# Kernel optimization log

Measured on AMD Instinct MI355X. Metric: run time of the kernel, lower is better.

## Reference

```python
import jax, jax.numpy as jnp
import numpy as np
import math

B, T, D, N = 4, 1024, 768, 7  # batch, seq, d_model, n_chambers
STEP, WARMUP = 4000, 2000      # curriculum: step past warmup -> all masks ~1
INIT_SCALE = 0.01


def _curriculum_masks():
    # NautilusScheduler.get_masks: smooth sigmoid activation per chamber (static floats)
    slope = 8.0 * N / WARMUP
    return [1.0 / (1.0 + math.exp(-slope * (STEP - WARMUP * (i + 0.5) / N))) for i in range(N)]


def _layernorm(x, g, b, eps=1e-5):
    m = jnp.mean(x, axis=-1, keepdims=True)
    v = jnp.mean((x - m) ** 2, axis=-1, keepdims=True)
    return (x - m) * jax.lax.rsqrt(v + eps) * g + b


def _chamber(h, Wq, Wk, gw, gb, sp, mask_val, causal):
    # get_bias stand-in: bilinear content bias (B,T,T)
    q = h @ Wq                                   # (B,T,D)
    k = h @ Wk                                   # (B,T,D)
    bias = jnp.einsum('btd,bsd->bts', q, k) / jnp.sqrt(jnp.asarray(D, h.dtype))
    bias = jnp.where(causal[None], bias, -jnp.inf)   # causal masked_fill
    w = jnp.nan_to_num(jax.nn.softmax(bias, axis=-1))
    enrichment = jnp.einsum('bts,bsd->btd', w, h) - h
    gate = jax.nn.sigmoid(h @ gw[:, None] + gb)      # (B,T,1)
    scale = jax.nn.softplus(sp)                      # learnable positive scale
    return scale * gate * mask_val * enrichment


def setup_inputs() -> dict:
    key = jax.random.key(0)
    ks = jax.random.split(key, 8)
    x = jax.random.normal(ks[0], (B, T, D), jnp.float32)
    s = 1.0 / np.sqrt(D)
    Wq = jax.random.normal(ks[1], (N, D, D), jnp.float32) * s
    Wk = jax.random.normal(ks[2], (N, D, D), jnp.float32) * s
    gate_w = jax.random.normal(ks[3], (N, D), jnp.float32) * 0.02
    gate_b = jnp.zeros((N,), jnp.float32)
    # per-chamber softplus-inverse init: log(exp(init*(1+3*prog))-1+1e-6)
    sp = np.array([math.log(math.exp(INIT_SCALE * (1.0 + 3.0 * i / (N - 1))) - 1.0 + 1e-6)
                   for i in range(N)], dtype=np.float32)
    scale_p = jnp.asarray(sp)
    merge_W = jax.random.normal(ks[4], (D, N * D), jnp.float32) * (1.0 / np.sqrt(N * D))
    return {
        'x': x, 'Wq': Wq, 'Wk': Wk, 'gate_w': gate_w, 'gate_b': gate_b,
        'scale_p': scale_p, 'merge_W': merge_W,
        'mode_logit': jnp.float32(0.0), 'residual_gate': jnp.float32(0.1),
        'ln_pre_g': jnp.ones((D,), jnp.float32), 'ln_pre_b': jnp.zeros((D,), jnp.float32),
        'ln_post_g': jnp.ones((D,), jnp.float32), 'ln_post_b': jnp.zeros((D,), jnp.float32),
    }


def reference(x, Wq, Wk, gate_w, gate_b, scale_p, merge_W, mode_logit,
              residual_gate, ln_pre_g, ln_pre_b, ln_post_g, ln_post_b):
    masks = _curriculum_masks()
    causal = jnp.tril(jnp.ones((T, T), bool))
    h = _layernorm(x, ln_pre_g, ln_pre_b)
    mode_gate = jax.nn.sigmoid(mode_logit)
    seq = jnp.zeros_like(h)
    deltas = []
    for i in range(N):  # fixed small structural loop over chambers
        seq = seq + _chamber(h + seq, Wq[i], Wk[i], gate_w[i], gate_b[i],
                             scale_p[i], masks[i], causal)
        deltas.append(_chamber(h, Wq[i], Wk[i], gate_w[i], gate_b[i],
                               scale_p[i], masks[i], causal))
    par = jnp.concatenate(deltas, axis=-1) @ merge_W.T  # (B,T,D)
    enrichment = (1.0 - mode_gate) * seq + mode_gate * par
    enrichment = _layernorm(enrichment, ln_post_g, ln_post_b)
    return x + residual_gate * enrichment
```

## Files before the change

### kernel.cpp

```cpp
#include <hip/hip_runtime.h>
#include <hip/hip_bf16.h>
#include <math.h>

#define D_MODEL 768
#define T_SEQ   1024
#define BATCH   4
#define NCH     7
#define ROWS    4096
#define KM      (NCH * D_MODEL)

typedef unsigned short u16;
typedef __attribute__((ext_vector_type(8))) short bh8;
typedef __attribute__((ext_vector_type(4))) float f32x4;

__device__ __forceinline__ u16 f2bf(float f) {
    union { float f; unsigned u; } v; v.f = f;
    return (u16)((v.u + 0x7fffu + ((v.u >> 16) & 1u)) >> 16);
}
__device__ __forceinline__ float bf2f(u16 b) {
    union { unsigned u; float f; } v; v.u = ((unsigned)b) << 16;
    return v.f;
}
__device__ __forceinline__ float wred_sum(float v) {
    #pragma unroll
    for (int o = 32; o; o >>= 1) v += __shfl_down(v, o, 64);
    return v;
}
__device__ __forceinline__ float wred_max(float v) {
    #pragma unroll
    for (int o = 32; o; o >>= 1) v = fmaxf(v, __shfl_down(v, o, 64));
    return v;
}
__device__ __forceinline__ float chamber_mask(int i) {
    float slope = 8.0f * 7.0f / 2000.0f;
    return 1.0f / (1.0f + __expf(-slope * (4000.0f - 2000.0f * (i + 0.5f) / 7.0f)));
}

#define GLD16(g, l) __builtin_amdgcn_global_load_lds( \
    (const __attribute__((address_space(1))) void*)(g), \
    (__attribute__((address_space(3))) void*)(l), 16, 0, 0)

__global__ __launch_bounds__(256)
void gemm_nt_kernel(const u16* __restrict__ A, const u16* __restrict__ B,
                    void* __restrict__ Cv,
                    int K, int lda, int ldb, int ldc,
                    long long sA1, long long sA2, long long sB1, long long sB2,
                    long long sC1, long long sC2, int zm,
                    float alpha, int mode, int causal_skip, int causal_k,
                    int kss, int klen)
{
    int bn = blockIdx.x, bm = blockIdx.y, bz = blockIdx.z;
    if (causal_skip && bn > bm) return;
    int bz1 = bz % zm, bz2 = bz / zm;

    const u16* Ab = A + bz1 * sA1 + bz2 * sA2 + (long long)(bm * 128) * lda;
    const u16* Bb = B + bz1 * sB1 + bz2 * sB2 + (long long)(bn * 128) * ldb;

    __shared__ u16 sm[4 * 128 * 32];
    u16* Al0 = sm;
    u16* Bl0 = sm + 128 * 32;
    u16* Al1 = sm + 2 * 128 * 32;
    u16* Bl1 = sm + 3 * 128 * 32;

    int tid  = threadIdx.x;
    int lane = tid & 63;
    int wave = tid >> 6;
    int wm = wave >> 1, wn = wave & 1;

    int k_begin = kss ? bz1 * kss : 0;
    int k_end   = klen ? (k_begin + klen) : K;
    if (causal_k) k_end = min(k_end, (bm + 1) * 128);

    f32x4 acc[4][4];
    #pragma unroll
    for (int i = 0; i < 4; i++)
        #pragma unroll
        for (int j = 0; j < 4; j++)
            acc[i][j] = (f32x4){0.f, 0.f, 0.f, 0.f};

    int srow = lane >> 2;
    int skq  = (lane & 3) * 8;
    int fm   = lane & 15;
    int fk   = (lane >> 4) * 8;

    for (int k0 = k_begin; k0 < k_end; k0 += 64) {
        __syncthreads();
        #pragma unroll
        for (int r = 0; r < 2; r++) {
            int row = r * 64 + wave * 16 + srow;
            long long ra = (long long)row * lda + k0 + skq;
            long long rb2 = (long long)row * ldb + k0 + skq;
            GLD16(Ab + ra,      Al0 + row * 32 + skq);
            GLD16(Bb + rb2,     Bl0 + row * 32 + skq);
            GLD16(Ab + ra + 32, Al1 + row * 32 + skq);
            GLD16(Bb + rb2 + 32, Bl1 + row * 32 + skq);
        }
        __syncthreads();

        #pragma unroll
        for (int p = 0; p < 2; p++) {
            const u16* Al = p ? Al1 : Al0;
            const u16* Bl = p ? Bl1 : Bl0;
            bh8 af[4], bf[4];
            #pragma unroll
            for (int i = 0; i < 4; i++)
                af[i] = *(const bh8*)(Al + (wm * 64 + i * 16 + fm) * 32 + fk);
            #pragma unroll
            for (int j = 0; j < 4; j++)
                bf[j] = *(const bh8*)(Bl + (wn * 64 + j * 16 + fm) * 32 + fk);
            #pragma unroll
            for (int i = 0; i < 4; i++)
                #pragma unroll
                for (int j = 0; j < 4; j++)
                    acc[i][j] = __builtin_amdgcn_mfma_f32_16x16x32_bf16(af[i], bf[j], acc[i][j], 0, 0, 0);
        }
    }

    int rbase = bm * 128 + wm * 64 + (lane >> 4) * 4;
    int cbase = bn * 128 + wn * 64 + (lane & 15);
    long long zoff = bz1 * sC1 + bz2 * sC2;
    if (mode == 1) {
        u16* C = (u16*)Cv + zoff;
        #pragma unroll
        for (int i = 0; i < 4; i++)
            #pragma unroll
            for (int j = 0; j < 4; j++)
                #pragma unroll
                for (int r = 0; r < 4; r++)
                    C[(long long)(rbase + i * 16 + r) * ldc + cbase + j * 16] = f2bf(acc[i][j][r] * alpha);
    } else if (mode == 3) {
        u16* C = (u16*)Cv + zoff;
        #pragma unroll
        for (int i = 0; i < 4; i++)
            #pragma unroll
            for (int j = 0; j < 4; j++)
                #pragma unroll
                for (int r = 0; r < 4; r++) {
                    union { _Float16 h; u16 u; } cv;
                    cv.h = (_Float16)(acc[i][j][r] * alpha);
                    C[(long long)(rbase + i * 16 + r) * ldc + cbase + j * 16] = cv.u;
                }
    } else {
        float* C = (float*)Cv + zoff;
        #pragma unroll
        for (int i = 0; i < 4; i++)
            #pragma unroll
            for (int j = 0; j < 4; j++)
                #pragma unroll
                for (int r = 0; r < 4; r++)
                    C[(long long)(rbase + i * 16 + r) * ldc + cbase + j * 16] = acc[i][j][r] * alpha;
    }
}

__global__ __launch_bounds__(256)
void gemm64_nt_kernel(const u16* __restrict__ A, const u16* __restrict__ B,
                      void* __restrict__ Cv,
                      int K, int lda, int ldb, int ldc,
                      long long sA1, long long sA2, long long sB1, long long sB2,
                      long long sC1, long long sC2, int zm,
                      float alpha, int mode, int causal_skip, int causal_k,
                      float* __restrict__ hhfp, const float* __restrict__ coefp,
                      u16* __restrict__ hbsp, u16* __restrict__ htsp,
                      const float* __restrict__ hp, u16* __restrict__ dbp)
{
    int bn = blockIdx.x, bm = blockIdx.y, bz = blockIdx.z;
    if (causal_skip && bn > bm) return;
    int bz1 = bz % zm, bz2 = bz / zm;

    const u16* Ab = A + bz1 * sA1 + bz2 * sA2 + (long long)(bm * 64) * lda;
    const u16* Bb = B + bz1 * sB1 + bz2 * sB2 + (long long)(bn * 64) * ldb;

    __shared__ u16 sm[4 * 64 * 32];
    u16* Al0 = sm;
    u16* Bl0 = sm + 64 * 32;
    u16* Al1 = sm + 2 * 64 * 32;
    u16* Bl1 = sm + 3 * 64 * 32;

    int tid  = threadIdx.x;
    int lane = tid & 63;
    int wave = tid >> 6;

    int k_end = causal_k ? min(K, (bm + 1) * 64) : K;

    f32x4 acc[4];
    #pragma unroll
    for (int j = 0; j < 4; j++) acc[j] = (f32x4){0.f, 0.f, 0.f, 0.f};

    int srow   = tid >> 2;
    int schunk = (tid & 3) * 8;
    int fm     = lane & 15;
    int fk     = (lane >> 4) * 8;

    for (int k0 = 0; k0 < k_end; k0 += 64) {
        __syncthreads();
        {
            long long ra  = (long long)srow * lda + k0 + schunk;
            long long rb2 = (long long)srow * ldb + k0 + schunk;
            GLD16(Ab + ra,       Al0 + srow * 32 + schunk);
            GLD16(Bb + rb2,      Bl0 + srow * 32 + schunk);
            GLD16(Ab + ra + 32,  Al1 + srow * 32 + schunk);
            GLD16(Bb + rb2 + 32, Bl1 + srow * 32 + schunk);
        }
        __syncthreads();

        #pragma unroll
        for (int p = 0; p < 2; p++) {
            const u16* Al = p ? Al1 : Al0;
            const u16* Bl = p ? Bl1 : Bl0;
            bh8 af = *(const bh8*)(Al + (wave * 16 + fm) * 32 + fk);
            bh8 bf[4];
            #pragma unroll
            for (int j = 0; j < 4; j++)
                bf[j] = *(const bh8*)(Bl + (j * 16 + fm) * 32 + fk);
            #pragma unroll
            for (int j = 0; j < 4; j++)
                acc[j] = __builtin_amdgcn_mfma_f32_16x16x32_bf16(af, bf[j], acc[j], 0, 0, 0);
        }
    }

    int rbase = bm * 64 + wave * 16 + (lane >> 4) * 4;
    int cbase = bn * 64 + (lane & 15);
    long long zoff = bz1 * sC1 + bz2 * sC2;
    if (mode == 1) {
        u16* C = (u16*)Cv + zoff;
        #pragma unroll
        for (int j = 0; j < 4; j++)
            #pragma unroll
            for (int r = 0; r < 4; r++)
                C[(long long)(rbase + r) * ldc + cbase + j * 16] = f2bf(acc[j][r] * alpha);
    } else if (mode == 3) {
        u16* C = (u16*)Cv + zoff;
        #pragma unroll
        for (int j = 0; j < 4; j++)
            #pragma unroll
            for (int r = 0; r < 4; r++) {
                union { _Float16 h; u16 u; } cv;
                cv.h = (_Float16)(acc[j][r] * alpha);
                C[(long long)(rbase + r) * ldc + cbase + j * 16] = cv.u;
            }
    } else if (mode == 5) {
        int b = bz1, ch = bz2;
        #pragma unroll
        for (int r = 0; r < 4; r++) {
            int t = rbase + r;
            long long rowg = (long long)b * T_SEQ + t;
            float cf = coefp[(long long)ch * ROWS + rowg];
            #pragma unroll
            for (int j = 0; j < 4; j++) {
                int d = cbase + j * 16;
                float hv = hp[rowg * D_MODEL + d];
                dbp[rowg * KM + ch * D_MODEL + d] = f2bf(cf * (acc[j][r] - hv));
            }
        }
    } else if (mode == 6) {
        __syncthreads();
        u16* tile = sm;
        #pragma unroll
        for (int r = 0; r < 4; r++) {
            int t = rbase + r;
            long long rowg = (long long)bz1 * T_SEQ + t;
            float cf = coefp[rowg];
            int tl = t - bm * 64;
            #pragma unroll
            for (int j = 0; j < 4; j++) {
                int d = cbase + j * 16;
                long long idx = rowg * D_MODEL + d;
                float v = hhfp[idx];
                float nh = v + cf * (acc[j][r] - v);
                hhfp[idx] = nh;
                u16 w = f2bf(nh);
                hbsp[idx] = w;
                tile[((lane & 15) + j * 16) * 66 + tl] = w;
            }
        }
        __syncthreads();
        int dl = tid >> 2, tch = (tid & 3) * 16;
        long long ob = (long long)bz1 * T_SEQ * D_MODEL +
                       (long long)(bn * 64 + dl) * T_SEQ + bm * 64 + tch;
        #pragma unroll
        for (int kk = 0; kk < 16; kk++)
            htsp[ob + kk] = tile[dl * 66 + tch + kk];
    } else {
        float* C = (float*)Cv + zoff;
        #pragma unroll
        for (int j = 0; j < 4; j++)
            #pragma unroll
            for (int r = 0; r < 4; r++)
                C[(long long)(rbase + r) * ldc + cbase + j * 16] = acc[j][r] * alpha;
    }
}

__global__ __launch_bounds__(256)
void ln_pre_kernel(const float* __restrict__ x, const float* __restrict__ g,
                   const float* __restrict__ b, float* __restrict__ h,
                   float* __restrict__ hhf, u16* __restrict__ hbp,
                   u16* __restrict__ hbs)
{
    int row = blockIdx.x;
    long long base = (long long)row * D_MODEL;
    int tid = threadIdx.x, lane = tid & 63, wave = tid >> 6;
    __shared__ float red[4];
    float v[3]; float s = 0.f;
    #pragma unroll
    for (int k = 0; k < 3; k++) { v[k] = x[base + tid + k * 256]; s += v[k]; }
    s = wred_sum(s);
    if (lane == 0) red[wave] = s;
    __syncthreads();
    float mean = (red[0] + red[1] + red[2] + red[3]) * (1.f / D_MODEL);
    __syncthreads();
    float sq = 0.f;
    #pragma unroll
    for (int k = 0; k < 3; k++) { float dd = v[k] - mean; sq += dd * dd; }
    sq = wred_sum(sq);
    if (lane == 0) red[wave] = sq;
    __syncthreads();
    float var = (red[0] + red[1] + red[2] + red[3]) * (1.f / D_MODEL);
    float rstd = rsqrtf(var + 1e-5f);
    #pragma unroll
    for (int k = 0; k < 3; k++) {
        int c = tid + k * 256;
        float o = (v[k] - mean) * rstd * g[c] + b[c];
        h[base + c] = o; hhf[base + c] = o;
        u16 w = f2bf(o);
        hbp[base + c] = w; hbs[base + c] = w;
    }
}

__global__ __launch_bounds__(256)
void transpose2_kernel(const u16* __restrict__ hb, u16* __restrict__ htp,
                       u16* __restrict__ hts)
{
    __shared__ u16 tile[32][33];
    int b = blockIdx.z;
    int d0 = blockIdx.x * 32, t0 = blockIdx.y * 32;
    int tx = threadIdx.x & 31, ty = threadIdx.x >> 5;
    long long bb = (long long)b * T_SEQ * D_MODEL;
    #pragma unroll
    for (int i = 0; i < 32; i += 8)
        tile[ty + i][tx] = hb[bb + (long long)(t0 + ty + i) * D_MODEL + d0 + tx];
    __syncthreads();
    #pragma unroll
    for (int i = 0; i < 32; i += 8) {
        long long o = bb + (long long)(d0 + ty + i) * T_SEQ + t0 + tx;
        u16 w = tile[tx][ty + i];
        htp[o] = w; hts[o] = w;
    }
}

__device__ __forceinline__ void softmax_row(u16* row, int len, int tid, int lane, int wave,
                                            float* red)
{
    float ev[4];
    float m = -3.0e38f;
    #pragma unroll
    for (int k = 0; k < 4; k++) {
        int s = tid + k * 256;
        if (s < len) {
            union { u16 u; _Float16 h; } cv; cv.u = row[s];
            ev[k] = (float)cv.h;
        } else ev[k] = -3.0e38f;
        m = fmaxf(m, ev[k]);
    }
    m = wred_max(m);
    if (lane == 0) red[wave] = m;
    __syncthreads();
    m = fmaxf(fmaxf(red[0], red[1]), fmaxf(red[2], red[3]));
    __syncthreads();
    float sum = 0.f;
    #pragma unroll
    for (int k = 0; k < 4; k++) {
        int s = tid + k * 256;
        float e = (s < len) ? __expf(ev[k] - m) : 0.f;
        ev[k] = e; sum += e;
    }
    sum = wred_sum(sum);
    if (lane == 0) red[wave] = sum;
    __syncthreads();
    sum = red[0] + red[1] + red[2] + red[3];
    float inv = 1.f / sum;
    #pragma unroll
    for (int k = 0; k < 4; k++)
        row[tid + k * 256] = f2bf(ev[k] * inv);
}

__global__ __launch_bounds__(256)
void softmax_kernel(u16* __restrict__ SP)
{
    int t = blockIdx.x, z = blockIdx.y;
    __shared__ float red[4];
    int tid = threadIdx.x, lane = tid & 63, wave = tid >> 6;
    softmax_row(SP + (long long)z * T_SEQ * T_SEQ + (long long)t * T_SEQ,
                t + 1, tid, lane, wave, red);
}

__global__ __launch_bounds__(256)
void softmax_coef_kernel(u16* __restrict__ SP, const float* __restrict__ hhf,
                         const float* __restrict__ gw, const float* __restrict__ gb,
                         const float* __restrict__ sp, int ci,
                         float* __restrict__ coefS)
{
    int t = blockIdx.x, z = blockIdx.y;
    int tid = threadIdx.x, lane = tid & 63, wave = tid >> 6;
    if (z == BATCH) {
        int row = t * 4 + wave;
        long long base = (long long)row * D_MODEL;
        const float* g = gw + ci * D_MODEL;
        float dot = 0.f;
        #pragma unroll
        for (int k = 0; k < 12; k++) dot += hhf[base + lane + 64 * k] * g[lane + 64 * k];
        dot = wred_sum(dot);
        if (lane == 0) {
            float gate = 1.f / (1.f + __expf(-(dot + gb[ci])));
            coefS[row] = log1pf(expf(sp[ci])) * chamber_mask(ci) * gate;
        }
        return;
    }
    __shared__ float red[4];
    softmax_row(SP + (long long)z * T_SEQ * T_SEQ + (long long)t * T_SEQ,
                t + 1, tid, lane, wave, red);
}

__global__ __launch_bounds__(256)
void coef_par_kernel(const float* __restrict__ h, const float* __restrict__ gw,
                     const float* __restrict__ gb, const float* __restrict__ sp,
                     float* __restrict__ coefP)
{
    int row = blockIdx.x * 4 + (threadIdx.x >> 6);
    int lane = threadIdx.x & 63;
    long long base = (long long)row * D_MODEL;
    float hv[12];
    #pragma unroll
    for (int k = 0; k < 12; k++) hv[k] = h[base + lane + 64 * k];
    for (int ci = 0; ci < NCH; ci++) {
        const float* g = gw + ci * D_MODEL;
        float dot = 0.f;
        #pragma unroll
        for (int k = 0; k < 12; k++) dot += hv[k] * g[lane + 64 * k];
        dot = wred_sum(dot);
        if (lane == 0) {
            float gate = 1.f / (1.f + __expf(-(dot + gb[ci])));
            coefP[ci * ROWS + row] = log1pf(expf(sp[ci])) * chamber_mask(ci) * gate;
        }
    }
}

__global__ __launch_bounds__(256)
void cast4_kernel(const float4* __restrict__ in, ushort4* __restrict__ outp, int n4)
{
    int i = blockIdx.x * 256 + threadIdx.x;
    if (i < n4) {
        float4 v = in[i];
        ushort4 o;
        o.x = f2bf(v.x); o.y = f2bf(v.y); o.z = f2bf(v.z); o.w = f2bf(v.w);
        outp[i] = o;
    }
}

__global__ __launch_bounds__(256)
void final_kernel(const float* __restrict__ x, const float* __restrict__ h,
                  const float* __restrict__ hhf, const u16* __restrict__ Pp,
                  const float* __restrict__ mode_logit, const float* __restrict__ residual_gate,
                  const float* __restrict__ g, const float* __restrict__ b,
                  float* __restrict__ out)
{
    const long long RDe = (long long)ROWS * D_MODEL;
    int row = blockIdx.x;
    long long base = (long long)row * D_MODEL;
    int tid = threadIdx.x, lane = tid & 63, wave = tid >> 6;
    __shared__ float red[4];
    float mg = 1.f / (1.f + __expf(-mode_logit[0]));
    float rg = residual_gate[0];
    float e[3]; float s = 0.f;
    #pragma unroll
    for (int k = 0; k < 3; k++) {
        int c = tid + k * 256;
        float p = 0.f;
        #pragma unroll
        for (int z = 0; z < NCH; z++) p += bf2f(Pp[z * RDe + base + c]);
        float v = (1.f - mg) * (hhf[base + c] - h[base + c]) + mg * p;
        e[k] = v; s += v;
    }
    s = wred_sum(s);
    if (lane == 0) red[wave] = s;
    __syncthreads();
    float mean = (red[0] + red[1] + red[2] + red[3]) * (1.f / D_MODEL);
    __syncthreads();
    float sq = 0.f;
    #pragma unroll
    for (int k = 0; k < 3; k++) { float dd = e[k] - mean; sq += dd * dd; }
    sq = wred_sum(sq);
    if (lane == 0) red[wave] = sq;
    __syncthreads();
    float var = (red[0] + red[1] + red[2] + red[3]) * (1.f / D_MODEL);
    float rstd = rsqrtf(var + 1e-5f);
    #pragma unroll
    for (int k = 0; k < 3; k++) {
        int c = tid + k * 256;
        out[base + c] = x[base + c] + rg * ((e[k] - mean) * rstd * g[c] + b[c]);
    }
}

extern "C" void kernel_launch(void* const* d_in, const int* in_sizes, int n_in,
                              void* d_out, int out_size, void* d_ws, size_t ws_size,
                              hipStream_t stream)
{
    (void)in_sizes; (void)n_in; (void)out_size; (void)ws_size;
    const float* x             = (const float*)d_in[0];
    const float* Wq            = (const float*)d_in[1];
    const float* Wk            = (const float*)d_in[2];
    const float* gate_w        = (const float*)d_in[3];
    const float* gate_b        = (const float*)d_in[4];
    const float* scale_p       = (const float*)d_in[5];
    const float* merge_W       = (const float*)d_in[6];
    const float* mode_logit    = (const float*)d_in[7];
    const float* residual_gate = (const float*)d_in[8];
    const float* ln_pre_g      = (const float*)d_in[9];
    const float* ln_pre_b      = (const float*)d_in[10];
    const float* ln_post_g     = (const float*)d_in[11];
    const float* ln_post_b     = (const float*)d_in[12];
    float* out = (float*)d_out;

    const long long DD  = (long long)D_MODEL * D_MODEL;
    const long long TD  = (long long)T_SEQ * D_MODEL;
    const long long TTs = (long long)T_SEQ * T_SEQ;
    const long long RDe = (long long)ROWS * D_MODEL;

    size_t off = 0;
    char* wsb = (char*)d_ws;
    auto alloc = [&](size_t bytes) -> void* {
        void* p = wsb + off; off += (bytes + 255) & ~(size_t)255; return p;
    };
    u16*   Mtb  = (u16*)alloc((size_t)NCH * DD * 2);
    u16*   mgb  = (u16*)alloc((size_t)D_MODEL * KM * 2);
    float* h    = (float*)alloc(RDe * 4);
    float* hhf  = (float*)alloc(RDe * 4);
    u16*   hbp  = (u16*)alloc(RDe * 2);
    u16*   htp  = (u16*)alloc(RDe * 2);
    u16*   hbs  = (u16*)alloc(RDe * 2);
    u16*   hts0 = (u16*)alloc(RDe * 2);
    u16*   hts1 = (u16*)alloc(RDe * 2);
    u16*   Spar = (u16*)alloc((size_t)(NCH * BATCH) * TTs * 2);
    u16*   Sseq = (u16*)alloc((size_t)BATCH * TTs * 2);
    u16*   Upar = (u16*)alloc((size_t)NCH * RDe * 2);
    u16*   Useq = (u16*)alloc(RDe * 2);
    u16*   db   = (u16*)alloc((size_t)ROWS * KM * 2);
    float* coefP= (float*)alloc((size_t)NCH * ROWS * 4);
    float* coefS= (float*)alloc((size_t)ROWS * 4);
    u16*   Wqb  = Spar;
    u16*   Wkb  = Spar + (size_t)NCH * DD;
    u16*   Pp   = Upar;

    const float sc = 1.0f / sqrtf((float)D_MODEL);
    const int N4W = (int)((size_t)NCH * DD) / 4;
    const int N4M = (int)((size_t)D_MODEL * KM) / 4;

    ln_pre_kernel<<<ROWS, 256, 0, stream>>>(x, ln_pre_g, ln_pre_b, h, hhf, hbp, hbs);
    cast4_kernel<<<(N4W + 255) / 256, 256, 0, stream>>>((const float4*)Wq, (ushort4*)Wqb, N4W);
    cast4_kernel<<<(N4W + 255) / 256, 256, 0, stream>>>((const float4*)Wk, (ushort4*)Wkb, N4W);
    cast4_kernel<<<(N4M + 255) / 256, 256, 0, stream>>>((const float4*)merge_W, (ushort4*)mgb, N4M);
    transpose2_kernel<<<dim3(24, 32, BATCH), 256, 0, stream>>>(hbp, htp, hts0);
    coef_par_kernel<<<ROWS / 4, 256, 0, stream>>>(h, gate_w, gate_b, scale_p, coefP);

    gemm_nt_kernel<<<dim3(6, 6, NCH), 256, 0, stream>>>(
        Wkb, Wqb, Mtb, D_MODEL, D_MODEL, D_MODEL, D_MODEL,
        DD, 0, DD, 0, DD, 0, NCH, 1.f, 1, 0, 0, 0, 0);

    gemm_nt_kernel<<<dim3(6, 32, NCH), 256, 0, stream>>>(
        hbp, Mtb, Upar, D_MODEL, D_MODEL, D_MODEL, D_MODEL,
        0, 0, DD, 0, RDe, 0, NCH, 1.f, 1, 0, 0, 0, 0);
    gemm64_nt_kernel<<<dim3(16, 16, BATCH * NCH), 256, 0, stream>>>(
        Upar, hbp, Spar, D_MODEL, D_MODEL, D_MODEL, T_SEQ,
        TD, RDe, TD, 0, TTs, 4 * TTs, BATCH, sc, 3, 1, 0,
        nullptr, nullptr, nullptr, nullptr, nullptr, nullptr);
    softmax_kernel<<<dim3(T_SEQ, BATCH * NCH), 256, 0, stream>>>(Spar);
    gemm64_nt_kernel<<<dim3(12, 16, BATCH * NCH), 256, 0, stream>>>(
        Spar, htp, nullptr, T_SEQ, T_SEQ, T_SEQ, D_MODEL,
        TTs, 4 * TTs, TD, 0, 0, 0, BATCH, 1.f, 5, 0, 1,
        nullptr, coefP, nullptr, nullptr, h, db);
    gemm_nt_kernel<<<dim3(6, 32, NCH), 256, 0, stream>>>(
        db, mgb, Pp, KM, KM, KM, D_MODEL,
        0, 0, 0, 0, RDe, 0, NCH, 1.f, 1, 0, 0, D_MODEL, D_MODEL);

    u16* htsCur = hts0;
    u16* htsNxt = hts1;
    for (int i = 0; i < NCH; i++) {
        gemm64_nt_kernel<<<dim3(12, 64, 1), 256, 0, stream>>>(
            hbs, Mtb + (long long)i * DD, Useq,
            D_MODEL, D_MODEL, D_MODEL, D_MODEL, 0, 0, 0, 0, 0, 0, 1,
            1.f, 1, 0, 0, nullptr, nullptr, nullptr, nullptr, nullptr, nullptr);
        gemm64_nt_kernel<<<dim3(16, 16, BATCH), 256, 0, stream>>>(
            Useq, hbs, Sseq, D_MODEL, D_MODEL, D_MODEL, T_SEQ,
            TD, 0, TD, 0, TTs, 0, BATCH, sc, 3, 1, 0,
            nullptr, nullptr, nullptr, nullptr, nullptr, nullptr);
        softmax_coef_kernel<<<dim3(T_SEQ, BATCH + 1), 256, 0, stream>>>(
            Sseq, hhf, gate_w, gate_b, scale_p, i, coefS);
        gemm64_nt_kernel<<<dim3(12, 16, BATCH), 256, 0, stream>>>(
            Sseq, htsCur, nullptr, T_SEQ, T_SEQ, T_SEQ, D_MODEL,
            TTs, 0, TD, 0, 0, 0, BATCH, 1.f, 6, 0, 1,
            hhf, coefS, hbs, htsNxt, nullptr, nullptr);
        u16* tmp = htsCur; htsCur = htsNxt; htsNxt = tmp;
    }

    final_kernel<<<ROWS, 256, 0, stream>>>(x, h, hhf, Pp, mode_logit, residual_gate,
                                           ln_post_g, ln_post_b, out);
}
```

Baseline: 907.9 us.

## Swizzle GEMM block order across XCDs and deepen K-step to 128

Both GEMM kernels now remap the flat block index so that consecutive blocks, which the hardware spreads across the 8 XCDs, end up working on contiguous tiles. This is meant to improve L2 locality per XCD. The 64-tile GEMM also loads 128 K-elements per barrier pair instead of 64, with a 64-wide tail path. That halves the synchronisation count but doubles shared memory per block, which may reduce occupancy. With causal block skipping, the swizzle also changes which early-exit blocks sit on which XCD.

```diff
diff --git a/kernel.cpp b/kernel.cpp
--- a/kernel.cpp
+++ b/kernel.cpp
@@ -39,6 +39,14 @@
 #define GLD16(g, l) __builtin_amdgcn_global_load_lds( \
     (const __attribute__((address_space(1))) void*)(g), \
     (__attribute__((address_space(3))) void*)(l), 16, 0, 0)
+
+__device__ __forceinline__ int xcd_swizzle(int gflat, int Ntot) {
+    if ((Ntot & 7) == 0) {
+        int chunk = Ntot >> 3;
+        gflat = (gflat & 7) * chunk + (gflat >> 3);
+    }
+    return gflat;
+}
 
 __global__ __launch_bounds__(256)
 void gemm_nt_kernel(const u16* __restrict__ A, const u16* __restrict__ B,
@@ -49,7 +57,13 @@
                     float alpha, int mode, int causal_skip, int causal_k,
                     int kss, int klen)
 {
-    int bn = blockIdx.x, bm = blockIdx.y, bz = blockIdx.z;
+    int gx = gridDim.x, gy = gridDim.y;
+    int Ntot = gx * gy * gridDim.z;
+    int gflat = xcd_swizzle(blockIdx.x + gx * (blockIdx.y + gy * blockIdx.z), Ntot);
+    int bn = gflat % gx;
+    int rest = gflat / gx;
+    int bm = rest % gy;
+    int bz = rest / gy;
     if (causal_skip && bn > bm) return;
     int bz1 = bz % zm, bz2 = bz / zm;
 
@@ -90,9 +104,9 @@
             int row = r * 64 + wave * 16 + srow;
             long long ra = (long long)row * lda + k0 + skq;
             long long rb2 = (long long)row * ldb + k0 + skq;
-            GLD16(Ab + ra,      Al0 + row * 32 + skq);
-            GLD16(Bb + rb2,     Bl0 + row * 32 + skq);
-            GLD16(Ab + ra + 32, Al1 + row * 32 + skq);
+            GLD16(Ab + ra,       Al0 + row * 32 + skq);
+            GLD16(Bb + rb2,      Bl0 + row * 32 + skq);
+            GLD16(Ab + ra + 32,  Al1 + row * 32 + skq);
             GLD16(Bb + rb2 + 32, Bl1 + row * 32 + skq);
         }
         __syncthreads();
@@ -163,18 +177,21 @@
                       u16* __restrict__ hbsp, u16* __restrict__ htsp,
                       const float* __restrict__ hp, u16* __restrict__ dbp)
 {
-    int bn = blockIdx.x, bm = blockIdx.y, bz = blockIdx.z;
+    int gx = gridDim.x, gy = gridDim.y;
+    int Ntot = gx * gy * gridDim.z;
+    int gflat = xcd_swizzle(blockIdx.x + gx * (blockIdx.y + gy * blockIdx.z), Ntot);
+    int bn = gflat % gx;
+    int rest = gflat / gx;
+    int bm = rest % gy;
+    int bz = rest / gy;
     if (causal_skip && bn > bm) return;
     int bz1 = bz % zm, bz2 = bz / zm;
 
     const u16* Ab = A + bz1 * sA1 + bz2 * sA2 + (long long)(bm * 64) * lda;
     const u16* Bb = B + bz1 * sB1 + bz2 * sB2 + (long long)(bn * 64) * ldb;
 
-    __shared__ u16 sm[4 * 64 * 32];
-    u16* Al0 = sm;
-    u16* Bl0 = sm + 64 * 32;
-    u16* Al1 = sm + 2 * 64 * 32;
-    u16* Bl1 = sm + 3 * 64 * 32;
+    __shared__ u16 sm[8 * 64 * 32];
+    const int PS = 64 * 32;
 
     int tid  = threadIdx.x;
     int lane = tid & 63;
@@ -191,30 +208,55 @@
     int fm     = lane & 15;
     int fk     = (lane >> 4) * 8;
 
-    for (int k0 = 0; k0 < k_end; k0 += 64) {
+    int k0 = 0;
+    while (k0 < k_end) {
         __syncthreads();
-        {
-            long long ra  = (long long)srow * lda + k0 + schunk;
-            long long rb2 = (long long)srow * ldb + k0 + schunk;
-            GLD16(Ab + ra,       Al0 + srow * 32 + schunk);
-            GLD16(Bb + rb2,      Bl0 + srow * 32 + schunk);
-            GLD16(Ab + ra + 32,  Al1 + srow * 32 + schunk);
-            GLD16(Bb + rb2 + 32, Bl1 + srow * 32 + schunk);
-        }
-        __syncthreads();
-
-        #pragma unroll
-        for (int p = 0; p < 2; p++) {
-            const u16* Al = p ? Al1 : Al0;
-            const u16* Bl = p ? Bl1 : Bl0;
-            bh8 af = *(const bh8*)(Al + (wave * 16 + fm) * 32 + fk);
-            bh8 bf[4];
-            #pragma unroll
-            for (int j = 0; j < 4; j++)
-                bf[j] = *(const bh8*)(Bl + (j * 16 + fm) * 32 + fk);
-            #pragma unroll
-            for (int j = 0; j < 4; j++)
-                acc[j] = __builtin_amdgcn_mfma_f32_16x16x32_bf16(af, bf[j], acc[j], 0, 0, 0);
+        if (k_end - k0 >= 128) {
+            #pragma unroll
+            for (int p = 0; p < 4; p++) {
+                long long ra  = (long long)srow * lda + k0 + p * 32 + schunk;
+                long long rb2 = (long long)srow * ldb + k0 + p * 32 + schunk;
+                GLD16(Ab + ra,  sm + (2 * p) * PS + srow * 32 + schunk);
+                GLD16(Bb + rb2, sm + (2 * p + 1) * PS + srow * 32 + schunk);
+            }
+            __syncthreads();
+            #pragma unroll
+            for (int p = 0; p < 4; p++) {
+                const u16* Al = sm + (2 * p) * PS;
+                const u16* Bl = sm + (2 * p + 1) * PS;
+                bh8 af = *(const bh8*)(Al + (wave * 16 + fm) * 32 + fk);
+                bh8 bf[4];
+                #pragma unroll
+                for (int j = 0; j < 4; j++)
+                    bf[j] = *(const bh8*)(Bl + (j * 16 + fm) * 32 + fk);
+                #pragma unroll
+                for (int j = 0; j < 4; j++)
+                    acc[j] = __builtin_amdgcn_mfma_f32_16x16x32_bf16(af, bf[j], acc[j], 0, 0, 0);
+            }
+            k0 += 128;
+        } else {
+            #pragma unroll
+            for (int p = 0; p < 2; p++) {
+                long long ra  = (long long)srow * lda + k0 + p * 32 + schunk;
+                long long rb2 = (long long)srow * ldb + k0 + p * 32 + schunk;
+                GLD16(Ab + ra,  sm + (2 * p) * PS + srow * 32 + schunk);
+                GLD16(Bb + rb2, sm + (2 * p + 1) * PS + srow * 32 + schunk);
+            }
+            __syncthreads();
+            #pragma unroll
+            for (int p = 0; p < 2; p++) {
+                const u16* Al = sm + (2 * p) * PS;
+                const u16* Bl = sm + (2 * p + 1) * PS;
+                bh8 af = *(const bh8*)(Al + (wave * 16 + fm) * 32 + fk);
+                bh8 bf[4];
+                #pragma unroll
+                for (int j = 0; j < 4; j++)
+                    bf[j] = *(const bh8*)(Bl + (j * 16 + fm) * 32 + fk);
+                #pragma unroll
+                for (int j = 0; j < 4; j++)
+                    acc[j] = __builtin_amdgcn_mfma_f32_16x16x32_bf16(af, bf[j], acc[j], 0, 0, 0);
+            }
+            k0 += 64;
         }
     }
 
```

New measurement: 790.7 us. 1.15x faster.
